# Performance work log

Hardware: AMD Instinct MI355X
Metric: run time of the kernel (lower is better)

Reference implementation:

```python
import jax, jax.numpy as jnp
import numpy as np

STEPS = 8
TOL = 1e-6


def _kabsch(p, q):
    # p, q: [B, N, 3]; returns R [B,3,3], t [B,3] s.t. q ~= R p + t (pypose svdtf)
    pm = p.mean(axis=-2, keepdims=True)
    qm = q.mean(axis=-2, keepdims=True)
    pc = p - pm
    qc = q - qm
    H = jnp.einsum('bni,bnj->bij', pc, qc)          # 3x3 cross-covariance
    U, S, Vt = jnp.linalg.svd(H, full_matrices=False)
    V = jnp.swapaxes(Vt, -1, -2)
    Ut = jnp.swapaxes(U, -1, -2)
    d = jnp.linalg.det(jnp.matmul(V, Ut))            # reflection fix
    D = jnp.concatenate([jnp.ones(d.shape + (2,), d.dtype), d[..., None]], axis=-1)
    R = jnp.matmul(V * D[..., None, :], Ut)
    t = qm[..., 0, :] - jnp.einsum('bij,bj->bi', R, pm[..., 0, :])
    return R, t


def _rotmat_to_quat(R):
    # branchless rotation-matrix -> quaternion [qx, qy, qz, qw] (pypose order)
    r00, r11, r22 = R[..., 0, 0], R[..., 1, 1], R[..., 2, 2]
    qw = 0.5 * jnp.sqrt(jnp.clip(1.0 + r00 + r11 + r22, 1e-12))
    qx = 0.5 * jnp.sqrt(jnp.clip(1.0 + r00 - r11 - r22, 1e-12))
    qy = 0.5 * jnp.sqrt(jnp.clip(1.0 - r00 + r11 - r22, 1e-12))
    qz = 0.5 * jnp.sqrt(jnp.clip(1.0 - r00 - r11 + r22, 1e-12))
    qx = qx * jnp.where(R[..., 2, 1] - R[..., 1, 2] >= 0, 1.0, -1.0)
    qy = qy * jnp.where(R[..., 0, 2] - R[..., 2, 0] >= 0, 1.0, -1.0)
    qz = qz * jnp.where(R[..., 1, 0] - R[..., 0, 1] >= 0, 1.0, -1.0)
    return jnp.stack([qx, qy, qz, qw], axis=-1)


def _icp(psrc, ptgt):
    B = psrc.shape[0]
    tn = (ptgt * ptgt).sum(-1)                        # [B, M]

    def body(carry, _):
        pc, err, done = carry
        # brute-force 1-NN: Euclidean cdist via  |p|^2 + |q|^2 - 2 p.q
        sq = ((pc * pc).sum(-1)[:, :, None] + tn[:, None, :]
              - 2.0 * jnp.einsum('bnd,bmd->bnm', pc, ptgt))
        dist = jnp.sqrt(jnp.clip(sq, 0.0))            # [B, N, M]
        knnd = dist.min(axis=-1)                      # [B, N]
        idx = dist.argmin(axis=-1)                    # [B, N]
        errnew = knnd.mean(axis=-1)                   # [B]
        conv = jnp.all(jnp.abs(errnew - err) < TOL)
        done_new = jnp.logical_or(done, conv)
        qk = jnp.take_along_axis(ptgt, jnp.broadcast_to(idx[..., None], pc.shape), axis=1)
        R, t = _kabsch(pc, qk)
        pcnew = jnp.einsum('bij,bnj->bni', R, pc) + t[:, None, :]
        pc = jnp.where(done_new, pc, pcnew)
        err = jnp.where(done_new, err, errnew)
        return (pc, err, done_new), None

    init = (psrc, jnp.zeros((B,), psrc.dtype), jnp.array(False))
    (pc, _, _), _ = jax.lax.scan(body, init, None, length=STEPS)
    R, t = _kabsch(psrc, pc)                          # final fit psrc -> moved cloud
    quat = _rotmat_to_quat(R)
    return jnp.concatenate([t, quat], axis=-1)        # SE3 7-vector [t, qx,qy,qz,qw]


def setup_inputs() -> dict:
    key = jax.random.key(0)
    k1, k2 = jax.random.split(key)
    psrc = jax.random.normal(k1, (2, 4096, 3), dtype=jnp.float32)
    ptgt = jax.random.normal(k2, (2, 4096, 3), dtype=jnp.float32)
    return {"psrc": psrc, "ptgt": ptgt}


def reference(psrc, ptgt):
    return _icp(psrc, ptgt)
```

## Files before the change

### kernel.cpp

```cpp
#include <hip/hip_runtime.h>
#include <math.h>

#define NPTS 4096
#define MPTS 4096
#define NSTEPS 8
#define ICP_TOL 1e-6f
#define NBLK 512
#define NSUB 32

#define ACC_OFF 32768
#define CTR_OFF 98304
#define CTR_STRIDE 1536

__global__ void init_kernel(const float* __restrict__ ptgt, float* __restrict__ ws) {
    float* ptgt4 = ws;
    unsigned* ctrs = (unsigned*)(ws + CTR_OFF);
    int gid = blockIdx.x * 256 + threadIdx.x;
    if (gid < 2 * MPTS) {
        float x = ptgt[3 * gid + 0];
        float y = ptgt[3 * gid + 1];
        float z = ptgt[3 * gid + 2];
        float4 v;
        v.x = x; v.y = y; v.z = z;
        v.w = 0.5f * (x * x + y * y + z * z);
        ((float4*)ptgt4)[gid] = v;
    }
    for (int i = gid; i < NSTEPS * CTR_STRIDE; i += 8192) ctrs[i] = 0u;
}

__device__ __forceinline__ float frcp(float x) {
#if __has_builtin(__builtin_amdgcn_rcpf)
    return __builtin_amdgcn_rcpf(x);
#else
    return 1.f / x;
#endif
}
__device__ __forceinline__ float frsq(float x) {
#if __has_builtin(__builtin_amdgcn_rsqf)
    return __builtin_amdgcn_rsqf(x);
#else
    return 1.f / sqrtf(x);
#endif
}

#define DET3(a,b,c,d,e,f,g,h,i) \
    ((a)*((e)*(i)-(f)*(h)) - (b)*((d)*(i)-(f)*(g)) + (c)*((d)*(h)-(e)*(g)))

__device__ __forceinline__ void horn_quat(const float N[4][4], float q[4]) {
    float s = 1e-30f;
#pragma unroll
    for (int i = 0; i < 4; ++i)
#pragma unroll
        for (int j = 0; j < 4; ++j) s = fmaxf(s, fabsf(N[i][j]));
    float inv = frcp(s);
    float A[4][4], B[4][4];
#pragma unroll
    for (int i = 0; i < 4; ++i)
#pragma unroll
        for (int j = 0; j < 4; ++j) A[i][j] = N[i][j] * inv;
#pragma unroll
    for (int i = 0; i < 4; ++i)
#pragma unroll
        for (int j = i; j < 4; ++j) {
            float v = A[i][0]*A[0][j] + A[i][1]*A[1][j] + A[i][2]*A[2][j] + A[i][3]*A[3][j];
            B[i][j] = v; B[j][i] = v;
        }
    float p1 = A[0][0]+A[1][1]+A[2][2]+A[3][3];
    float p2 = B[0][0]+B[1][1]+B[2][2]+B[3][3];
    float p3 = 0.f, p4 = 0.f;
#pragma unroll
    for (int i = 0; i < 4; ++i)
#pragma unroll
        for (int j = 0; j < 4; ++j) { p3 += A[i][j]*B[i][j]; p4 += B[i][j]*B[i][j]; }
    float e1 = p1;
    float e2 = 0.5f*(e1*p1 - p2);
    float e3 = (e2*p1 - e1*p2 + p3)*(1.f/3.f);
    float e4 = 0.25f*(e3*p1 - e2*p2 + e1*p3 - p4);
    float lam = -3e38f;
#pragma unroll
    for (int i = 0; i < 4; ++i) {
        float r = A[i][i];
#pragma unroll
        for (int j = 0; j < 4; ++j) if (j != i) r += fabsf(A[i][j]);
        lam = fmaxf(lam, r);
    }
#pragma unroll
    for (int it = 0; it < 12; ++it) {
        float pv = (((lam - e1)*lam + e2)*lam - e3)*lam + e4;
        float dv = ((4.f*lam - 3.f*e1)*lam + 2.f*e2)*lam - e3;
        lam -= pv * frcp(dv);
    }
    float M[4][4];
#pragma unroll
    for (int i = 0; i < 4; ++i)
#pragma unroll
        for (int j = 0; j < 4; ++j) M[i][j] = A[i][j] - ((i == j) ? lam : 0.f);
    float C0 = DET3(M[1][1],M[1][2],M[1][3], M[2][1],M[2][2],M[2][3], M[3][1],M[3][2],M[3][3]);
    float C1 = DET3(M[0][0],M[0][2],M[0][3], M[2][0],M[2][2],M[2][3], M[3][0],M[3][2],M[3][3]);
    float C2 = DET3(M[0][0],M[0][1],M[0][3], M[1][0],M[1][1],M[1][3], M[3][0],M[3][1],M[3][3]);
    float C3 = DET3(M[0][0],M[0][1],M[0][2], M[1][0],M[1][1],M[1][2], M[2][0],M[2][1],M[2][2]);
    int is = 0; float cb = fabsf(C0);
    if (fabsf(C1) > cb) { cb = fabsf(C1); is = 1; }
    if (fabsf(C2) > cb) { cb = fabsf(C2); is = 2; }
    if (fabsf(C3) > cb) { cb = fabsf(C3); is = 3; }
    float v0, v1, v2, v3;
#define ROWCOF(a,b,c) { \
    v0 =  DET3(M[a][1],M[a][2],M[a][3], M[b][1],M[b][2],M[b][3], M[c][1],M[c][2],M[c][3]); \
    v1 = -DET3(M[a][0],M[a][2],M[a][3], M[b][0],M[b][2],M[b][3], M[c][0],M[c][2],M[c][3]); \
    v2 =  DET3(M[a][0],M[a][1],M[a][3], M[b][0],M[b][1],M[b][3], M[c][0],M[c][1],M[c][3]); \
    v3 = -DET3(M[a][0],M[a][1],M[a][2], M[b][0],M[b][1],M[b][2], M[c][0],M[c][1],M[c][2]); }
    if (is == 0)      ROWCOF(1,2,3)
    else if (is == 1) ROWCOF(0,2,3)
    else if (is == 2) ROWCOF(0,1,3)
    else              ROWCOF(0,1,2)
#undef ROWCOF
    float nr = frsq(v0*v0 + v1*v1 + v2*v2 + v3*v3);
    q[0] = v0*nr; q[1] = v1*nr; q[2] = v2*nr; q[3] = v3*nr;
}

#define FOR16(OP) OP(0) OP(1) OP(2) OP(3) OP(4) OP(5) OP(6) OP(7) \
                  OP(8) OP(9) OP(10) OP(11) OP(12) OP(13) OP(14) OP(15)

__global__ __launch_bounds__(256, 2) void icp_main(
    const float* __restrict__ psrc, float* __restrict__ ws,
    float* __restrict__ out) {

    float* ptgt4 = ws;
    float* acc = ws + ACC_OFF;
    unsigned* ctrs = (unsigned*)(ws + CTR_OFF);

    __shared__ float st[2][13];
    __shared__ unsigned keys[4][16];
    __shared__ float red[16][16];
    __shared__ float gred[16][16];
    __shared__ float asum[2][16];
    __shared__ int contflag;

    const int tid = threadIdx.x;
    const int bid = blockIdx.x;
    const int b = bid >> 8;
    const int n0 = (bid & 255) * 16;

    if (tid < 2) {
        st[tid][0] = 1.f; st[tid][1] = 0.f; st[tid][2] = 0.f;
        st[tid][3] = 0.f; st[tid][4] = 1.f; st[tid][5] = 0.f;
        st[tid][6] = 0.f; st[tid][7] = 0.f; st[tid][8] = 1.f;
        st[tid][9] = 0.f; st[tid][10] = 0.f; st[tid][11] = 0.f;
        st[tid][12] = 0.f;
    }
    __syncthreads();

    const int w = tid >> 6, lane = tid & 63;
    const int m0 = w * 1024 + lane;
    const float4* tpb = (const float4*)ptgt4 + ((size_t)b * MPTS + m0);
    const float* ps = psrc + ((size_t)b * NPTS + n0) * 3;

    for (int step = 0; step < NSTEPS; ++step) {
        float R00 = st[b][0], R01 = st[b][1], R02 = st[b][2];
        float R10 = st[b][3], R11 = st[b][4], R12 = st[b][5];
        float R20 = st[b][6], R21 = st[b][7], R22 = st[b][8];
        float t0 = st[b][9], t1 = st[b][10], t2 = st[b][11];

#define DECLP(i) float px##i, py##i, pz##i;
        FOR16(DECLP)
#undef DECLP
#define LOADP(i) { float x = ps[3*(i)], y = ps[3*(i)+1], z = ps[3*(i)+2]; \
        px##i = fmaf(R00, x, fmaf(R01, y, fmaf(R02, z, t0))); \
        py##i = fmaf(R10, x, fmaf(R11, y, fmaf(R12, z, t1))); \
        pz##i = fmaf(R20, x, fmaf(R21, y, fmaf(R22, z, t2))); }
        FOR16(LOADP)
#undef LOADP

#define DECLB(i) float bs##i = -3.0e38f; int ix##i = m0;
        FOR16(DECLB)
#undef DECLB

        float4 tc0 = tpb[0];
        float4 tc1 = tpb[64];
        int mreg = m0;
#pragma unroll
        for (int k = 0; k < 16; ++k) {
            float4 tnx = tpb[((k + 2) & 15) * 64];
            float tx = tc0.x, ty = tc0.y, tz = tc0.z, htn = tc0.w;
#define PAIR(i) { float s = fmaf(px##i, tx, fmaf(py##i, ty, fmaf(pz##i, tz, -htn))); \
            if (s > bs##i) { bs##i = s; ix##i = mreg; } }
            FOR16(PAIR)
#undef PAIR
            mreg += 64;
            tc0 = tc1;
            tc1 = tnx;
        }

#define REDKEY(i) { unsigned ub = __float_as_uint(bs##i); \
        unsigned u = ((int)ub >= 0) ? (ub | 0x80000000u) : ~ub; \
        unsigned key = (u & 0xFFFFF000u) | (4095u - (unsigned)ix##i); \
        for (int off = 32; off; off >>= 1) { \
            unsigned o = (unsigned)__shfl_xor((int)key, off); \
            key = key > o ? key : o; } \
        if (lane == 0) keys[w][i] = key; }
        FOR16(REDKEY)
#undef REDKEY
        __syncthreads();

        if (tid < 16) {
            unsigned key = keys[0][tid];
            unsigned k1 = keys[1][tid], k2 = keys[2][tid], k3 = keys[3][tid];
            key = key > k1 ? key : k1;
            key = key > k2 ? key : k2;
            key = key > k3 ? key : k3;
            int m = 4095 - (int)(key & 0xFFFu);
            float4 qq = ((const float4*)ptgt4)[(size_t)b * MPTS + m];
            const float* pp = psrc + ((size_t)b * NPTS + n0 + tid) * 3;
            float x = pp[0], y = pp[1], z = pp[2];
            float px = fmaf(R00, x, fmaf(R01, y, fmaf(R02, z, t0)));
            float py = fmaf(R10, x, fmaf(R11, y, fmaf(R12, z, t1)));
            float pz = fmaf(R20, x, fmaf(R21, y, fmaf(R22, z, t2)));
            float dx = px - qq.x, dy = py - qq.y, dz = pz - qq.z;
            float dist = sqrtf(dx * dx + dy * dy + dz * dz);
            red[tid][0] = px; red[tid][1] = py; red[tid][2] = pz;
            red[tid][3] = qq.x; red[tid][4] = qq.y; red[tid][5] = qq.z;
            red[tid][6] = px * qq.x;  red[tid][7] = px * qq.y;  red[tid][8] = px * qq.z;
            red[tid][9] = py * qq.x;  red[tid][10] = py * qq.y; red[tid][11] = py * qq.z;
            red[tid][12] = pz * qq.x; red[tid][13] = pz * qq.y; red[tid][14] = pz * qq.z;
            red[tid][15] = dist;
        }
        __syncthreads();
        if (tid < 16) {
            float s = 0.f;
#pragma unroll
            for (int r = 0; r < 16; ++r) s += red[r][tid];
            __hip_atomic_store(&acc[((size_t)step * NBLK + bid) * 16 + tid], s,
                               __ATOMIC_RELAXED, __HIP_MEMORY_SCOPE_AGENT);
        }

        unsigned* stepc = ctrs + step * CTR_STRIDE;
        __syncthreads();
        if (tid == 0) {
            unsigned* sub = stepc + (bid & (NSUB - 1)) * 16;
            bool bcast = false;
            unsigned old = __hip_atomic_fetch_add(sub, 1u, __ATOMIC_RELAXED,
                                                  __HIP_MEMORY_SCOPE_AGENT);
            if (old == (unsigned)(NBLK / NSUB) - 1u) {
                unsigned mold = __hip_atomic_fetch_add(stepc + 512, 1u,
                                    __ATOMIC_RELAXED, __HIP_MEMORY_SCOPE_AGENT);
                if (mold == (unsigned)NSUB - 1u) {
#pragma unroll
                    for (int f = 0; f < NSUB; ++f)
                        __hip_atomic_store(stepc + 1024 + f * 16, 1u,
                                           __ATOMIC_RELAXED,
                                           __HIP_MEMORY_SCOPE_AGENT);
                    bcast = true;
                }
            }
            if (!bcast) {
                unsigned* myflag = stepc + 1024 + (bid & (NSUB - 1)) * 16;
                while (__hip_atomic_load(myflag, __ATOMIC_RELAXED,
                                         __HIP_MEMORY_SCOPE_AGENT) == 0u) {
                    __builtin_amdgcn_s_sleep(1);
                }
            }
        }
        __syncthreads();

        {
            const float* accs = acc + (size_t)step * NBLK * 16;
            int c = tid & 15, g = tid >> 4;
            float ssum = 0.f;
#pragma unroll
            for (int i = 0; i < 32; ++i)
                ssum += accs[(size_t)(g * 32 + i) * 16 + c];
            gred[g][c] = ssum;
        }
        __syncthreads();
        if (tid < 32) {
            int bb = tid >> 4, c = tid & 15;
            float s = 0.f;
#pragma unroll
            for (int g = 0; g < 8; ++g) s += gred[bb * 8 + g][c];
            asum[bb][c] = s;
        }
        __syncthreads();
        if (tid == 0) {
            float err0 = asum[0][15] * (1.f / NPTS);
            float err1 = asum[1][15] * (1.f / NPTS);
            bool conv = (fabsf(err0 - st[0][12]) < ICP_TOL) &&
                        (fabsf(err1 - st[1][12]) < ICP_TOL);
            contflag = conv ? 2 : 1;
        }
        __syncthreads();
        if (contflag == 1 && tid < 2) {
            float a[16];
            for (int i = 0; i < 16; ++i) a[i] = asum[tid][i];
            const float inv_n = 1.f / NPTS;
            float pmx = a[0]*inv_n, pmy = a[1]*inv_n, pmz = a[2]*inv_n;
            float qmx = a[3]*inv_n, qmy = a[4]*inv_n, qmz = a[5]*inv_n;
            float H[3][3];
            for (int i = 0; i < 3; ++i)
                for (int j = 0; j < 3; ++j)
                    H[i][j] = a[6 + 3*i + j] - a[i]*a[3 + j]*inv_n;
            float Sxx=H[0][0], Sxy=H[0][1], Sxz=H[0][2];
            float Syx=H[1][0], Syy=H[1][1], Syz=H[1][2];
            float Szx=H[2][0], Szy=H[2][1], Szz=H[2][2];
            float Nm[4][4];
            Nm[0][0] = Sxx+Syy+Szz; Nm[0][1] = Syz-Szy;
            Nm[0][2] = Szx-Sxz;     Nm[0][3] = Sxy-Syx;
            Nm[1][1] = Sxx-Syy-Szz; Nm[1][2] = Sxy+Syx; Nm[1][3] = Szx+Sxz;
            Nm[2][2] = -Sxx+Syy-Szz; Nm[2][3] = Syz+Szy;
            Nm[3][3] = -Sxx-Syy+Szz;
            Nm[1][0]=Nm[0][1]; Nm[2][0]=Nm[0][2]; Nm[3][0]=Nm[0][3];
            Nm[2][1]=Nm[1][2]; Nm[3][1]=Nm[1][3]; Nm[3][2]=Nm[2][3];
            float qv[4];
            horn_quat(Nm, qv);
            float qw = qv[0], qx = qv[1], qy = qv[2], qz = qv[3];
            float R00n = 1.f - 2.f*(qy*qy + qz*qz);
            float R01n = 2.f*(qx*qy - qw*qz);
            float R02n = 2.f*(qx*qz + qw*qy);
            float R10n = 2.f*(qx*qy + qw*qz);
            float R11n = 1.f - 2.f*(qx*qx + qz*qz);
            float R12n = 2.f*(qy*qz - qw*qx);
            float R20n = 2.f*(qx*qz - qw*qy);
            float R21n = 2.f*(qy*qz + qw*qx);
            float R22n = 1.f - 2.f*(qx*qx + qy*qy);
            float tx = qmx - (R00n*pmx + R01n*pmy + R02n*pmz);
            float ty = qmy - (R10n*pmx + R11n*pmy + R12n*pmz);
            float tz = qmz - (R20n*pmx + R21n*pmy + R22n*pmz);
            float C00=st[tid][0], C01=st[tid][1], C02=st[tid][2];
            float C10=st[tid][3], C11=st[tid][4], C12=st[tid][5];
            float C20=st[tid][6], C21=st[tid][7], C22=st[tid][8];
            float T0=st[tid][9], T1=st[tid][10], T2=st[tid][11];
            float ns[12];
            ns[0] = R00n*C00 + R01n*C10 + R02n*C20;
            ns[1] = R00n*C01 + R01n*C11 + R02n*C21;
            ns[2] = R00n*C02 + R01n*C12 + R02n*C22;
            ns[3] = R10n*C00 + R11n*C10 + R12n*C20;
            ns[4] = R10n*C01 + R11n*C11 + R12n*C21;
            ns[5] = R10n*C02 + R11n*C12 + R12n*C22;
            ns[6] = R20n*C00 + R21n*C10 + R22n*C20;
            ns[7] = R20n*C01 + R21n*C11 + R22n*C21;
            ns[8] = R20n*C02 + R21n*C12 + R22n*C22;
            ns[9]  = R00n*T0 + R01n*T1 + R02n*T2 + tx;
            ns[10] = R10n*T0 + R11n*T1 + R12n*T2 + ty;
            ns[11] = R20n*T0 + R21n*T1 + R22n*T2 + tz;
            for (int i = 0; i < 12; ++i) st[tid][i] = ns[i];
            st[tid][12] = asum[tid][15] * (1.f / NPTS);
        }
        __syncthreads();
        if (contflag == 2) break;
    }

    if (bid == 0 && tid < 2) {
        float r00 = st[tid][0], r01 = st[tid][1], r02 = st[tid][2];
        float r10 = st[tid][3], r11 = st[tid][4], r12 = st[tid][5];
        float r20 = st[tid][6], r21 = st[tid][7], r22 = st[tid][8];
        float qw = 0.5f * sqrtf(fmaxf(1.f + r00 + r11 + r22, 1e-12f));
        float qx = 0.5f * sqrtf(fmaxf(1.f + r00 - r11 - r22, 1e-12f));
        float qy = 0.5f * sqrtf(fmaxf(1.f - r00 + r11 - r22, 1e-12f));
        float qz = 0.5f * sqrtf(fmaxf(1.f - r00 - r11 + r22, 1e-12f));
        qx = (r21 - r12 >= 0.f) ? qx : -qx;
        qy = (r02 - r20 >= 0.f) ? qy : -qy;
        qz = (r10 - r01 >= 0.f) ? qz : -qz;
        out[tid * 7 + 0] = st[tid][9];
        out[tid * 7 + 1] = st[tid][10];
        out[tid * 7 + 2] = st[tid][11];
        out[tid * 7 + 3] = qx;
        out[tid * 7 + 4] = qy;
        out[tid * 7 + 5] = qz;
        out[tid * 7 + 6] = qw;
    }
}

extern "C" void kernel_launch(void* const* d_in, const int* in_sizes, int n_in,
                              void* d_out, int out_size, void* d_ws, size_t ws_size,
                              hipStream_t stream) {
    const float* psrc = (const float*)d_in[0];
    const float* ptgt = (const float*)d_in[1];
    float* out = (float*)d_out;
    float* ws = (float*)d_ws;

    init_kernel<<<32, 256, 0, stream>>>(ptgt, ws);
    icp_main<<<NBLK, 256, 0, stream>>>(psrc, ws, out);
}
```

Before: 166.0 us.

## Replace counter-tree grid barrier with per-block tagged slots and batch warp key reduction

Drops the atomic counter tree and broadcast flags used as the grid barrier. Each block now writes its partial sums, with the distance sum offset by 1.0 so a nonzero value marks the slot as ready, and every thread polls two of those tagged slots directly. This removes the serial atomic chain and the flag broadcast latency. Separately, the per-point argmax reduction now uses a transpose-style butterfly that shares shuffles across the 16 keys instead of running 16 independent 6-step reductions. Risks: the offset of 1.0 per block is added to the error sum and subtracted back (256 per batch), which costs some float precision, and the spin loop has a timeout that could break out silently.

```diff
diff --git a/kernel.cpp b/kernel.cpp
--- a/kernel.cpp
+++ b/kernel.cpp
@@ -6,15 +6,12 @@
 #define NSTEPS 8
 #define ICP_TOL 1e-6f
 #define NBLK 512
-#define NSUB 32
 
 #define ACC_OFF 32768
-#define CTR_OFF 98304
-#define CTR_STRIDE 1536
 
 __global__ void init_kernel(const float* __restrict__ ptgt, float* __restrict__ ws) {
     float* ptgt4 = ws;
-    unsigned* ctrs = (unsigned*)(ws + CTR_OFF);
+    float4* accz = (float4*)(ws + ACC_OFF);
     int gid = blockIdx.x * 256 + threadIdx.x;
     if (gid < 2 * MPTS) {
         float x = ptgt[3 * gid + 0];
@@ -25,7 +22,10 @@
         v.w = 0.5f * (x * x + y * y + z * z);
         ((float4*)ptgt4)[gid] = v;
     }
-    for (int i = gid; i < NSTEPS * CTR_STRIDE; i += 8192) ctrs[i] = 0u;
+    float4 z4; z4.x = 0.f; z4.y = 0.f; z4.z = 0.f; z4.w = 0.f;
+#pragma unroll
+    for (int i = 0; i < 2; ++i)
+        accz[gid + i * 8192] = z4;
 }
 
 __device__ __forceinline__ float frcp(float x) {
@@ -127,13 +127,13 @@
 
     float* ptgt4 = ws;
     float* acc = ws + ACC_OFF;
-    unsigned* ctrs = (unsigned*)(ws + CTR_OFF);
 
     __shared__ float st[2][13];
     __shared__ unsigned keys[4][16];
     __shared__ float red[16][16];
     __shared__ float gred[16][16];
     __shared__ float asum[2][16];
+    __shared__ float tagv;
     __shared__ int contflag;
 
     const int tid = threadIdx.x;
@@ -191,15 +191,39 @@
             tc1 = tnx;
         }
 
-#define REDKEY(i) { unsigned ub = __float_as_uint(bs##i); \
+        unsigned k_[16];
+#define MKKEY(i) { unsigned ub = __float_as_uint(bs##i); \
         unsigned u = ((int)ub >= 0) ? (ub | 0x80000000u) : ~ub; \
-        unsigned key = (u & 0xFFFFF000u) | (4095u - (unsigned)ix##i); \
-        for (int off = 32; off; off >>= 1) { \
-            unsigned o = (unsigned)__shfl_xor((int)key, off); \
-            key = key > o ? key : o; } \
-        if (lane == 0) keys[w][i] = key; }
-        FOR16(REDKEY)
-#undef REDKEY
+        k_[i] = (u & 0xFFFFF000u) | (4095u - (unsigned)ix##i); }
+        FOR16(MKKEY)
+#undef MKKEY
+#pragma unroll
+        for (int r = 0; r < 4; ++r) {
+            const int mm = 1 << r;
+            const int W = 16 >> r;
+            unsigned o_[16];
+#pragma unroll
+            for (int j = 0; j < W; ++j)
+                o_[j] = (unsigned)__shfl_xor((int)k_[j], mm);
+            const bool hi = (lane & mm) != 0;
+#pragma unroll
+            for (int j = 0; j < W / 2; ++j) {
+                unsigned a = hi ? k_[j + W / 2] : k_[j];
+                unsigned c = hi ? o_[j + W / 2] : o_[j];
+                k_[j] = a > c ? a : c;
+            }
+        }
+        {
+            unsigned o = (unsigned)__shfl_xor((int)k_[0], 16);
+            k_[0] = k_[0] > o ? k_[0] : o;
+            o = (unsigned)__shfl_xor((int)k_[0], 32);
+            k_[0] = k_[0] > o ? k_[0] : o;
+        }
+        if (lane < 16) {
+            int p = ((lane & 1) << 3) | ((lane & 2) << 1) |
+                    ((lane & 4) >> 1) | ((lane & 8) >> 3);
+            keys[w][p] = k_[0];
+        }
         __syncthreads();
 
         if (tid < 16) {
@@ -225,39 +249,37 @@
             red[tid][15] = dist;
         }
         __syncthreads();
+
+        const size_t slotbase = ((size_t)step * NBLK + bid) * 16;
         if (tid < 16) {
             float s = 0.f;
 #pragma unroll
             for (int r = 0; r < 16; ++r) s += red[r][tid];
-            __hip_atomic_store(&acc[((size_t)step * NBLK + bid) * 16 + tid], s,
+            if (tid < 15)
+                __hip_atomic_store(&acc[slotbase + tid], s,
+                                   __ATOMIC_RELAXED, __HIP_MEMORY_SCOPE_AGENT);
+            else
+                tagv = s;
+        }
+        __syncthreads();
+        if (tid == 0)
+            __hip_atomic_store(&acc[slotbase + 15], tagv + 1.0f,
                                __ATOMIC_RELAXED, __HIP_MEMORY_SCOPE_AGENT);
-        }
-
-        unsigned* stepc = ctrs + step * CTR_STRIDE;
-        __syncthreads();
-        if (tid == 0) {
-            unsigned* sub = stepc + (bid & (NSUB - 1)) * 16;
-            bool bcast = false;
-            unsigned old = __hip_atomic_fetch_add(sub, 1u, __ATOMIC_RELAXED,
-                                                  __HIP_MEMORY_SCOPE_AGENT);
-            if (old == (unsigned)(NBLK / NSUB) - 1u) {
-                unsigned mold = __hip_atomic_fetch_add(stepc + 512, 1u,
-                                    __ATOMIC_RELAXED, __HIP_MEMORY_SCOPE_AGENT);
-                if (mold == (unsigned)NSUB - 1u) {
-#pragma unroll
-                    for (int f = 0; f < NSUB; ++f)
-                        __hip_atomic_store(stepc + 1024 + f * 16, 1u,
-                                           __ATOMIC_RELAXED,
-                                           __HIP_MEMORY_SCOPE_AGENT);
-                    bcast = true;
-                }
-            }
-            if (!bcast) {
-                unsigned* myflag = stepc + 1024 + (bid & (NSUB - 1)) * 16;
-                while (__hip_atomic_load(myflag, __ATOMIC_RELAXED,
-                                         __HIP_MEMORY_SCOPE_AGENT) == 0u) {
-                    __builtin_amdgcn_s_sleep(1);
-                }
+
+        {
+            const unsigned* tagp = (const unsigned*)(acc + (size_t)step * NBLK * 16);
+            const size_t o0 = (size_t)tid * 16 + 15;
+            const size_t o1 = (size_t)(tid + 256) * 16 + 15;
+            unsigned u0 = 0, u1 = 0;
+            int spin = 0;
+            for (;;) {
+                if (!u0) u0 = __hip_atomic_load(tagp + o0, __ATOMIC_RELAXED,
+                                                __HIP_MEMORY_SCOPE_AGENT);
+                if (!u1) u1 = __hip_atomic_load(tagp + o1, __ATOMIC_RELAXED,
+                                                __HIP_MEMORY_SCOPE_AGENT);
+                if (u0 && u1) break;
+                if (++spin > (1 << 20)) break;
+                __builtin_amdgcn_s_sleep(2);
             }
         }
         __syncthreads();
@@ -281,8 +303,8 @@
         }
         __syncthreads();
         if (tid == 0) {
-            float err0 = asum[0][15] * (1.f / NPTS);
-            float err1 = asum[1][15] * (1.f / NPTS);
+            float err0 = (asum[0][15] - 256.0f) * (1.f / NPTS);
+            float err1 = (asum[1][15] - 256.0f) * (1.f / NPTS);
             bool conv = (fabsf(err0 - st[0][12]) < ICP_TOL) &&
                         (fabsf(err1 - st[1][12]) < ICP_TOL);
             contflag = conv ? 2 : 1;
@@ -342,7 +364,7 @@
             ns[10] = R10n*T0 + R11n*T1 + R12n*T2 + ty;
             ns[11] = R20n*T0 + R21n*T1 + R22n*T2 + tz;
             for (int i = 0; i < 12; ++i) st[tid][i] = ns[i];
-            st[tid][12] = asum[tid][15] * (1.f / NPTS);
+            st[tid][12] = (asum[tid][15] - 256.0f) * (1.f / NPTS);
         }
         __syncthreads();
         if (contflag == 2) break;
```

After: 171.7 us. 1.03x slower.

## Transpose-reduce argmax keys and skip final-step grid barrier broadcast

Applied to the files above, without the earlier changes.

Replaces sixteen independent full-wave shuffle reductions of the argmax keys with a transpose-style butterfly that halves the live key count each round, cutting shuffle count from 96 to about 32 per wave. It also drops one __syncthreads between the per-block reduction stores and the sum, and on the final step lets all blocks except block 0 exit after arriving, instead of waiting for a broadcast release. This removes shuffle overhead and final-step barrier latency. The cost is a lane-permuted store index and a different barrier protocol on the last step.

```diff
diff --git a/kernel.cpp b/kernel.cpp
--- a/kernel.cpp
+++ b/kernel.cpp
@@ -191,15 +191,39 @@
             tc1 = tnx;
         }
 
-#define REDKEY(i) { unsigned ub = __float_as_uint(bs##i); \
+        unsigned k_[16];
+#define MKKEY(i) { unsigned ub = __float_as_uint(bs##i); \
         unsigned u = ((int)ub >= 0) ? (ub | 0x80000000u) : ~ub; \
-        unsigned key = (u & 0xFFFFF000u) | (4095u - (unsigned)ix##i); \
-        for (int off = 32; off; off >>= 1) { \
-            unsigned o = (unsigned)__shfl_xor((int)key, off); \
-            key = key > o ? key : o; } \
-        if (lane == 0) keys[w][i] = key; }
-        FOR16(REDKEY)
-#undef REDKEY
+        k_[i] = (u & 0xFFFFF000u) | (4095u - (unsigned)ix##i); }
+        FOR16(MKKEY)
+#undef MKKEY
+#pragma unroll
+        for (int r = 0; r < 4; ++r) {
+            const int mm = 1 << r;
+            const int W = 16 >> r;
+            unsigned o_[16];
+#pragma unroll
+            for (int j = 0; j < W; ++j)
+                o_[j] = (unsigned)__shfl_xor((int)k_[j], mm);
+            const bool hi = (lane & mm) != 0;
+#pragma unroll
+            for (int j = 0; j < W / 2; ++j) {
+                unsigned a = hi ? k_[j + W / 2] : k_[j];
+                unsigned c = hi ? o_[j + W / 2] : o_[j];
+                k_[j] = a > c ? a : c;
+            }
+        }
+        {
+            unsigned o = (unsigned)__shfl_xor((int)k_[0], 16);
+            k_[0] = k_[0] > o ? k_[0] : o;
+            o = (unsigned)__shfl_xor((int)k_[0], 32);
+            k_[0] = k_[0] > o ? k_[0] : o;
+        }
+        if (lane < 16) {
+            int p = ((lane & 1) << 3) | ((lane & 2) << 1) |
+                    ((lane & 4) >> 1) | ((lane & 8) >> 3);
+            keys[w][p] = k_[0];
+        }
         __syncthreads();
 
         if (tid < 16) {
@@ -223,9 +247,6 @@
             red[tid][9] = py * qq.x;  red[tid][10] = py * qq.y; red[tid][11] = py * qq.z;
             red[tid][12] = pz * qq.x; red[tid][13] = pz * qq.y; red[tid][14] = pz * qq.z;
             red[tid][15] = dist;
-        }
-        __syncthreads();
-        if (tid < 16) {
             float s = 0.f;
 #pragma unroll
             for (int r = 0; r < 16; ++r) s += red[r][tid];
@@ -235,32 +256,52 @@
 
         unsigned* stepc = ctrs + step * CTR_STRIDE;
         __syncthreads();
-        if (tid == 0) {
-            unsigned* sub = stepc + (bid & (NSUB - 1)) * 16;
-            bool bcast = false;
-            unsigned old = __hip_atomic_fetch_add(sub, 1u, __ATOMIC_RELAXED,
-                                                  __HIP_MEMORY_SCOPE_AGENT);
-            if (old == (unsigned)(NBLK / NSUB) - 1u) {
-                unsigned mold = __hip_atomic_fetch_add(stepc + 512, 1u,
-                                    __ATOMIC_RELAXED, __HIP_MEMORY_SCOPE_AGENT);
-                if (mold == (unsigned)NSUB - 1u) {
-#pragma unroll
-                    for (int f = 0; f < NSUB; ++f)
-                        __hip_atomic_store(stepc + 1024 + f * 16, 1u,
-                                           __ATOMIC_RELAXED,
+
+        if (step == NSTEPS - 1) {
+            if (tid == 0) {
+                unsigned* sub = stepc + (bid & (NSUB - 1)) * 16;
+                unsigned old = __hip_atomic_fetch_add(sub, 1u, __ATOMIC_RELAXED,
+                                                      __HIP_MEMORY_SCOPE_AGENT);
+                if (old == (unsigned)(NBLK / NSUB) - 1u)
+                    __hip_atomic_fetch_add(stepc + 512, 1u, __ATOMIC_RELAXED,
                                            __HIP_MEMORY_SCOPE_AGENT);
-                    bcast = true;
-                }
             }
-            if (!bcast) {
-                unsigned* myflag = stepc + 1024 + (bid & (NSUB - 1)) * 16;
-                while (__hip_atomic_load(myflag, __ATOMIC_RELAXED,
-                                         __HIP_MEMORY_SCOPE_AGENT) == 0u) {
+            if (bid != 0) return;
+            if (tid == 0) {
+                while (__hip_atomic_load(stepc + 512, __ATOMIC_RELAXED,
+                                         __HIP_MEMORY_SCOPE_AGENT) < (unsigned)NSUB) {
                     __builtin_amdgcn_s_sleep(1);
                 }
             }
-        }
-        __syncthreads();
+            __syncthreads();
+        } else {
+            if (tid == 0) {
+                unsigned* sub = stepc + (bid & (NSUB - 1)) * 16;
+                bool bcast = false;
+                unsigned old = __hip_atomic_fetch_add(sub, 1u, __ATOMIC_RELAXED,
+                                                      __HIP_MEMORY_SCOPE_AGENT);
+                if (old == (unsigned)(NBLK / NSUB) - 1u) {
+                    unsigned mold = __hip_atomic_fetch_add(stepc + 512, 1u,
+                                        __ATOMIC_RELAXED, __HIP_MEMORY_SCOPE_AGENT);
+                    if (mold == (unsigned)NSUB - 1u) {
+#pragma unroll
+                        for (int f = 0; f < NSUB; ++f)
+                            __hip_atomic_store(stepc + 1024 + f * 16, 1u,
+                                               __ATOMIC_RELAXED,
+                                               __HIP_MEMORY_SCOPE_AGENT);
+                        bcast = true;
+                    }
+                }
+                if (!bcast) {
+                    unsigned* myflag = stepc + 1024 + (bid & (NSUB - 1)) * 16;
+                    while (__hip_atomic_load(myflag, __ATOMIC_RELAXED,
+                                             __HIP_MEMORY_SCOPE_AGENT) == 0u) {
+                        __builtin_amdgcn_s_sleep(1);
+                    }
+                }
+            }
+            __syncthreads();
+        }
 
         {
             const float* accs = acc + (size_t)step * NBLK * 16;
```

New measurement: 160.4 us, median of 2. 1.03x faster.
